# Kernel tuning notes

Measured on AMD Instinct MI355X. Metric: run time of the kernel, lower is better.

## Reference

```python
import jax, jax.numpy as jnp
import numpy as np

B, I, O = 8192, 512, 512

def setup_inputs() -> dict:
    key = jax.random.key(0)
    k1, k2, k3, k4 = jax.random.split(key, 4)
    x = jax.random.normal(k1, (B, I), dtype=jnp.float32)
    # per-edge polynomial activation params: f_ij(t) = w1*t + w2*t^2 + w3*t^3 + b
    edge_w = jax.random.normal(k2, (I, O, 3), dtype=jnp.float32) * 0.1
    edge_b = jax.random.normal(k3, (I, O), dtype=jnp.float32) * 0.1
    # xavier-uniform combination weights
    limit = float(np.sqrt(6.0 / (I + O)))
    comb_w = jax.random.uniform(k4, (I, O), dtype=jnp.float32, minval=-limit, maxval=limit)
    return {"x": x, "edge_w": edge_w, "edge_b": edge_b, "comb_w": comb_w}

def reference(x, edge_w, edge_b, comb_w):
    # basis: [B, I, 3] = (t, t^2, t^3)
    basis = jnp.stack([x, x * x, x * x * x], axis=-1)
    # out[b,o] = sum_i comb_w[i,o] * (sum_k basis[b,i,k]*edge_w[i,o,k] + edge_b[i,o])
    # fused to avoid materializing [B, I, O]
    w_eff = edge_w * comb_w[:, :, None]            # [I, O, 3]
    out = jnp.einsum('bik,iok->bo', basis, w_eff)  # [B, O]
    out = out + jnp.sum(comb_w * edge_b, axis=0)   # bias term, [O]
    return out
```

## Files before the change

kernel.cpp:

```cpp
#include <hip/hip_runtime.h>
#include <hip/hip_bf16.h>
#include <stdint.h>


static constexpr int ON_ = 512;

typedef __bf16 bf16x8 __attribute__((ext_vector_type(8)));
typedef float  f32x4  __attribute__((ext_vector_type(4)));

__device__ __forceinline__ unsigned int f2bf(float f) {
    unsigned int u = __float_as_uint(f);
    return ((u + 0x7FFFu + ((u >> 16) & 1u)) >> 16);
}

__global__ __launch_bounds__(256) void pack_all(const float* __restrict__ x,
                                                const float* __restrict__ edge_w,
                                                const float* __restrict__ comb_w,
                                                const float* __restrict__ edge_b,
                                                uint4* __restrict__ Xpk,
                                                uint4* __restrict__ Bpk,
                                                float* __restrict__ bias) {
    int bb = blockIdx.x;
    if (bb < 2048) {
        int id = bb * 256 + threadIdx.x;
        int l  = id & 63;
        int w  = id >> 6;
        int g  = w & 15;
        int rb = w >> 4;
        int r  = rb * 16 + (l & 15);
        int c  = g * 32 + ((l >> 4) << 3);
        const float4* xp = (const float4*)(x + (size_t)r * 512 + c);
        float4 v0 = xp[0], v1 = xp[1];
        uint4 o;
        o.x = f2bf(v0.x) | (f2bf(v0.y) << 16);
        o.y = f2bf(v0.z) | (f2bf(v0.w) << 16);
        o.z = f2bf(v1.x) | (f2bf(v1.y) << 16);
        o.w = f2bf(v1.z) | (f2bf(v1.w) << 16);
        Xpk[(size_t)w * 64 + l] = o;
    } else if (bb < 2176) {
        int id = (bb - 2048) * 256 + threadIdx.x;
        int l  = id & 63;
        int t  = id >> 6;
        int g  = t & 15;
        int cb = t >> 4;
        int o  = cb * 16 + (l & 15);
        int i0 = g * 32 + ((l >> 4) << 3);
        unsigned int w[3][4];
#pragma unroll
        for (int j = 0; j < 4; ++j) {
            int ia = i0 + 2 * j, ic = ia + 1;
            float ca = comb_w[(size_t)ia * ON_ + o];
            float cc = comb_w[(size_t)ic * ON_ + o];
            const float* ea = edge_w + ((size_t)ia * ON_ + o) * 3;
            const float* ec = edge_w + ((size_t)ic * ON_ + o) * 3;
#pragma unroll
            for (int p = 0; p < 3; ++p)
                w[p][j] = f2bf(ea[p] * ca) | (f2bf(ec[p] * cc) << 16);
        }
        size_t base = ((size_t)cb * 48 + g * 3) * 64 + l;
        Bpk[base]       = make_uint4(w[0][0], w[0][1], w[0][2], w[0][3]);
        Bpk[base + 64]  = make_uint4(w[1][0], w[1][1], w[1][2], w[1][3]);
        Bpk[base + 128] = make_uint4(w[2][0], w[2][1], w[2][2], w[2][3]);
    } else {
        __shared__ float red[4][64];
        int bo = bb - 2176;
        int tt = threadIdx.x;
        int o  = bo * 64 + (tt & 63);
        int iseg = tt >> 6;
        float s = 0.f;
        int ib = iseg * 128;
#pragma unroll 4
        for (int i = ib; i < ib + 128; ++i)
            s += comb_w[(size_t)i * ON_ + o] * edge_b[(size_t)i * ON_ + o];
        red[iseg][tt & 63] = s;
        __syncthreads();
        if (tt < 64)
            bias[bo * 64 + tt] = red[0][tt] + red[1][tt] + red[2][tt] + red[3][tt];
    }
}

#define PM(CAm, MI, CB0_, CB1_, CB2_, CB3_, CB4_, CB5_) do {                           \
    bf16x8 a1_ = __builtin_bit_cast(bf16x8, (CAm));                                    \
    float e0_ = __uint_as_float((CAm).x << 16), e1_ = __uint_as_float((CAm).x & 0xffff0000u); \
    float e2_ = __uint_as_float((CAm).y << 16), e3_ = __uint_as_float((CAm).y & 0xffff0000u); \
    float e4_ = __uint_as_float((CAm).z << 16), e5_ = __uint_as_float((CAm).z & 0xffff0000u); \
    float e6_ = __uint_as_float((CAm).w << 16), e7_ = __uint_as_float((CAm).w & 0xffff0000u); \
    float q0_ = e0_*e0_, q1_ = e1_*e1_, q2_ = e2_*e2_, q3_ = e3_*e3_;                  \
    float q4_ = e4_*e4_, q5_ = e5_*e5_, q6_ = e6_*e6_, q7_ = e7_*e7_;                  \
    bf16x8 a2_ = (bf16x8){ (__bf16)q0_, (__bf16)q1_, (__bf16)q2_, (__bf16)q3_,         \
                           (__bf16)q4_, (__bf16)q5_, (__bf16)q6_, (__bf16)q7_ };       \
    bf16x8 a3_ = (bf16x8){ (__bf16)(q0_*e0_), (__bf16)(q1_*e1_), (__bf16)(q2_*e2_), (__bf16)(q3_*e3_), \
                           (__bf16)(q4_*e4_), (__bf16)(q5_*e5_), (__bf16)(q6_*e6_), (__bf16)(q7_*e7_) }; \
    acc[MI][0] = __builtin_amdgcn_mfma_f32_16x16x32_bf16(a1_, __builtin_bit_cast(bf16x8, CB0_), acc[MI][0], 0, 0, 0); \
    acc[MI][1] = __builtin_amdgcn_mfma_f32_16x16x32_bf16(a1_, __builtin_bit_cast(bf16x8, CB3_), acc[MI][1], 0, 0, 0); \
    acc[MI][0] = __builtin_amdgcn_mfma_f32_16x16x32_bf16(a2_, __builtin_bit_cast(bf16x8, CB1_), acc[MI][0], 0, 0, 0); \
    acc[MI][1] = __builtin_amdgcn_mfma_f32_16x16x32_bf16(a2_, __builtin_bit_cast(bf16x8, CB4_), acc[MI][1], 0, 0, 0); \
    acc[MI][0] = __builtin_amdgcn_mfma_f32_16x16x32_bf16(a3_, __builtin_bit_cast(bf16x8, CB2_), acc[MI][0], 0, 0, 0); \
    acc[MI][1] = __builtin_amdgcn_mfma_f32_16x16x32_bf16(a3_, __builtin_bit_cast(bf16x8, CB5_), acc[MI][1], 0, 0, 0); \
} while (0)

#define STEP(PREF, CA0,CA1,CA2,CA3, CB0,CB1,CB2,CB3,CB4,CB5,                           \
                   NA0,NA1,NA2,NA3, NB0,NB1,NB2,NB3,NB4,NB5, WAITS) do {               \
    if (PREF) {                                                                        \
        NA0 = *(const uint4*)(pa0); NA1 = *(const uint4*)(pa1);                        \
        NA2 = *(const uint4*)(pa2); NA3 = *(const uint4*)(pa3);                        \
        NB0 = *(const uint4*)(pb0);        NB1 = *(const uint4*)(pb0 + 1024);          \
        NB2 = *(const uint4*)(pb0 + 2048); NB3 = *(const uint4*)(pb1);                 \
        NB4 = *(const uint4*)(pb1 + 1024); NB5 = *(const uint4*)(pb1 + 2048);          \
        pa0 += 1024; pa1 += 1024; pa2 += 1024; pa3 += 1024;                            \
        pb0 += 3072; pb1 += 3072;                                                      \
    }                                                                                  \
    asm volatile("s_waitcnt " WAITS ::: "memory");                                     \
    PM(CA0, 0, CB0, CB1, CB2, CB3, CB4, CB5);                                          \
    PM(CA1, 1, CB0, CB1, CB2, CB3, CB4, CB5);                                          \
    PM(CA2, 2, CB0, CB1, CB2, CB3, CB4, CB5);                                          \
    PM(CA3, 3, CB0, CB1, CB2, CB3, CB4, CB5);                                          \
} while (0)

__global__ __launch_bounds__(256, 2) void gemm_fused(const char* __restrict__ Xpk,
                                                     const char* __restrict__ Bpk,
                                                     const float* __restrict__ bias,
                                                     float* __restrict__ out) {
    const int tid = threadIdx.x;
    const int l   = tid & 63;
    const int wid = tid >> 6;
    const int wr  = wid >> 1, wc = wid & 1;

    int d  = blockIdx.x;
    int w  = (d & 7) * 64 + (d >> 3);
    int bx = w >> 3, by = w & 7;

    const char* pa0 = Xpk + ((size_t)(bx * 8 + wr * 4) * 16) * 1024 + (l << 4);
    const char* pa1 = pa0 + 16 * 1024;
    const char* pa2 = pa0 + 32 * 1024;
    const char* pa3 = pa0 + 48 * 1024;
    const char* pb0 = Bpk + ((size_t)(by * 4 + wc * 2) * 48) * 1024 + (l << 4);
    const char* pb1 = pb0 + 48 * 1024;

    f32x4 acc[4][2] = {};
    uint4 cA0, cA1, cA2, cA3, cB0, cB1, cB2, cB3, cB4, cB5;
    uint4 nA0, nA1, nA2, nA3, nB0, nB1, nB2, nB3, nB4, nB5;

    cA0 = *(const uint4*)(pa0); cA1 = *(const uint4*)(pa1);
    cA2 = *(const uint4*)(pa2); cA3 = *(const uint4*)(pa3);
    cB0 = *(const uint4*)(pb0);        cB1 = *(const uint4*)(pb0 + 1024);
    cB2 = *(const uint4*)(pb0 + 2048); cB3 = *(const uint4*)(pb1);
    cB4 = *(const uint4*)(pb1 + 1024); cB5 = *(const uint4*)(pb1 + 2048);
    pa0 += 1024; pa1 += 1024; pa2 += 1024; pa3 += 1024;
    pb0 += 3072; pb1 += 3072;

    for (int gp = 0; gp < 7; ++gp) {
        STEP(true, cA0,cA1,cA2,cA3, cB0,cB1,cB2,cB3,cB4,cB5,
                   nA0,nA1,nA2,nA3, nB0,nB1,nB2,nB3,nB4,nB5, "vmcnt(10)");
        STEP(true, nA0,nA1,nA2,nA3, nB0,nB1,nB2,nB3,nB4,nB5,
                   cA0,cA1,cA2,cA3, cB0,cB1,cB2,cB3,cB4,cB5, "vmcnt(10)");
    }
    STEP(true,  cA0,cA1,cA2,cA3, cB0,cB1,cB2,cB3,cB4,cB5,
                nA0,nA1,nA2,nA3, nB0,nB1,nB2,nB3,nB4,nB5, "vmcnt(10)");
    STEP(false, nA0,nA1,nA2,nA3, nB0,nB1,nB2,nB3,nB4,nB5,
                cA0,cA1,cA2,cA3, cB0,cB1,cB2,cB3,cB4,cB5, "vmcnt(0)");

    int lr = l >> 4, lc = l & 15;
#pragma unroll
    for (int n = 0; n < 2; ++n) {
        int o = (by << 6) + (wc << 5) + (n << 4) + lc;
        float bv = bias[o];
#pragma unroll
        for (int m = 0; m < 4; ++m) {
            int r0 = (bx << 7) + (wr << 6) + (m << 4) + (lr << 2);
#pragma unroll
            for (int j = 0; j < 4; ++j)
                out[(size_t)(r0 + j) * ON_ + o] = acc[m][n][j] + bv;
        }
    }
}

extern "C" void kernel_launch(void* const* d_in, const int* in_sizes, int n_in,
                              void* d_out, int out_size, void* d_ws, size_t ws_size,
                              hipStream_t stream) {
    const float* x      = (const float*)d_in[0];
    const float* edge_w = (const float*)d_in[1];
    const float* edge_b = (const float*)d_in[2];
    const float* comb_w = (const float*)d_in[3];
    float* out = (float*)d_out;

    char* ws = (char*)d_ws;
    char* Xpk   = ws;
    char* Bpk   = ws + 8388608;
    float* bias = (float*)(ws + 8388608 + 1572864);

    hipLaunchKernelGGL(pack_all, dim3(2048 + 128 + 8), dim3(256), 0, stream,
                       x, edge_w, comb_w, edge_b, (uint4*)Xpk, (uint4*)Bpk, bias);
    hipLaunchKernelGGL(gemm_fused, dim3(512), dim3(256), 0, stream, Xpk, Bpk, bias, out);
}
```

Measured before the change: 40.43 us.

## Deepen GEMM prefetch to triple-buffered registers and reorder MFMA issue

```diff
diff --git a/kernel.cpp b/kernel.cpp
--- a/kernel.cpp
+++ b/kernel.cpp
@@ -79,43 +79,66 @@
     }
 }
 
-#define PM(CAm, MI, CB0_, CB1_, CB2_, CB3_, CB4_, CB5_) do {                           \
-    bf16x8 a1_ = __builtin_bit_cast(bf16x8, (CAm));                                    \
-    float e0_ = __uint_as_float((CAm).x << 16), e1_ = __uint_as_float((CAm).x & 0xffff0000u); \
-    float e2_ = __uint_as_float((CAm).y << 16), e3_ = __uint_as_float((CAm).y & 0xffff0000u); \
-    float e4_ = __uint_as_float((CAm).z << 16), e5_ = __uint_as_float((CAm).z & 0xffff0000u); \
-    float e6_ = __uint_as_float((CAm).w << 16), e7_ = __uint_as_float((CAm).w & 0xffff0000u); \
-    float q0_ = e0_*e0_, q1_ = e1_*e1_, q2_ = e2_*e2_, q3_ = e3_*e3_;                  \
-    float q4_ = e4_*e4_, q5_ = e5_*e5_, q6_ = e6_*e6_, q7_ = e7_*e7_;                  \
-    bf16x8 a2_ = (bf16x8){ (__bf16)q0_, (__bf16)q1_, (__bf16)q2_, (__bf16)q3_,         \
-                           (__bf16)q4_, (__bf16)q5_, (__bf16)q6_, (__bf16)q7_ };       \
-    bf16x8 a3_ = (bf16x8){ (__bf16)(q0_*e0_), (__bf16)(q1_*e1_), (__bf16)(q2_*e2_), (__bf16)(q3_*e3_), \
-                           (__bf16)(q4_*e4_), (__bf16)(q5_*e5_), (__bf16)(q6_*e6_), (__bf16)(q7_*e7_) }; \
-    acc[MI][0] = __builtin_amdgcn_mfma_f32_16x16x32_bf16(a1_, __builtin_bit_cast(bf16x8, CB0_), acc[MI][0], 0, 0, 0); \
-    acc[MI][1] = __builtin_amdgcn_mfma_f32_16x16x32_bf16(a1_, __builtin_bit_cast(bf16x8, CB3_), acc[MI][1], 0, 0, 0); \
-    acc[MI][0] = __builtin_amdgcn_mfma_f32_16x16x32_bf16(a2_, __builtin_bit_cast(bf16x8, CB1_), acc[MI][0], 0, 0, 0); \
-    acc[MI][1] = __builtin_amdgcn_mfma_f32_16x16x32_bf16(a2_, __builtin_bit_cast(bf16x8, CB4_), acc[MI][1], 0, 0, 0); \
-    acc[MI][0] = __builtin_amdgcn_mfma_f32_16x16x32_bf16(a3_, __builtin_bit_cast(bf16x8, CB2_), acc[MI][0], 0, 0, 0); \
-    acc[MI][1] = __builtin_amdgcn_mfma_f32_16x16x32_bf16(a3_, __builtin_bit_cast(bf16x8, CB5_), acc[MI][1], 0, 0, 0); \
+__device__ __forceinline__ void ext_sq(const uint4 a, float* e, float* q) {
+    e[0] = __uint_as_float(a.x << 16); e[1] = __uint_as_float(a.x & 0xffff0000u);
+    e[2] = __uint_as_float(a.y << 16); e[3] = __uint_as_float(a.y & 0xffff0000u);
+    e[4] = __uint_as_float(a.z << 16); e[5] = __uint_as_float(a.z & 0xffff0000u);
+    e[6] = __uint_as_float(a.w << 16); e[7] = __uint_as_float(a.w & 0xffff0000u);
+#pragma unroll
+    for (int i = 0; i < 8; ++i) q[i] = e[i] * e[i];
+}
+
+#define MFMA_ROW(F0, F1, F2, F3, BN0, BN1) do {                                           \
+    bf16x8 b0_ = __builtin_bit_cast(bf16x8, BN0);                                         \
+    bf16x8 b1_ = __builtin_bit_cast(bf16x8, BN1);                                         \
+    acc[0][0] = __builtin_amdgcn_mfma_f32_16x16x32_bf16(F0, b0_, acc[0][0], 0, 0, 0);      \
+    acc[1][0] = __builtin_amdgcn_mfma_f32_16x16x32_bf16(F1, b0_, acc[1][0], 0, 0, 0);      \
+    acc[2][0] = __builtin_amdgcn_mfma_f32_16x16x32_bf16(F2, b0_, acc[2][0], 0, 0, 0);      \
+    acc[3][0] = __builtin_amdgcn_mfma_f32_16x16x32_bf16(F3, b0_, acc[3][0], 0, 0, 0);      \
+    acc[0][1] = __builtin_amdgcn_mfma_f32_16x16x32_bf16(F0, b1_, acc[0][1], 0, 0, 0);      \
+    acc[1][1] = __builtin_amdgcn_mfma_f32_16x16x32_bf16(F1, b1_, acc[1][1], 0, 0, 0);      \
+    acc[2][1] = __builtin_amdgcn_mfma_f32_16x16x32_bf16(F2, b1_, acc[2][1], 0, 0, 0);      \
+    acc[3][1] = __builtin_amdgcn_mfma_f32_16x16x32_bf16(F3, b1_, acc[3][1], 0, 0, 0);      \
 } while (0)
 
-#define STEP(PREF, CA0,CA1,CA2,CA3, CB0,CB1,CB2,CB3,CB4,CB5,                           \
-                   NA0,NA1,NA2,NA3, NB0,NB1,NB2,NB3,NB4,NB5, WAITS) do {               \
-    if (PREF) {                                                                        \
-        NA0 = *(const uint4*)(pa0); NA1 = *(const uint4*)(pa1);                        \
-        NA2 = *(const uint4*)(pa2); NA3 = *(const uint4*)(pa3);                        \
-        NB0 = *(const uint4*)(pb0);        NB1 = *(const uint4*)(pb0 + 1024);          \
-        NB2 = *(const uint4*)(pb0 + 2048); NB3 = *(const uint4*)(pb1);                 \
-        NB4 = *(const uint4*)(pb1 + 1024); NB5 = *(const uint4*)(pb1 + 2048);          \
-        pa0 += 1024; pa1 += 1024; pa2 += 1024; pa3 += 1024;                            \
-        pb0 += 3072; pb1 += 3072;                                                      \
-    }                                                                                  \
-    asm volatile("s_waitcnt " WAITS ::: "memory");                                     \
-    PM(CA0, 0, CB0, CB1, CB2, CB3, CB4, CB5);                                          \
-    PM(CA1, 1, CB0, CB1, CB2, CB3, CB4, CB5);                                          \
-    PM(CA2, 2, CB0, CB1, CB2, CB3, CB4, CB5);                                          \
-    PM(CA3, 3, CB0, CB1, CB2, CB3, CB4, CB5);                                          \
+#define COMP(A0, A1, A2, A3, B0, B1, B2, B3, B4, B5) do {                                  \
+    bf16x8 f0_ = __builtin_bit_cast(bf16x8, A0), f1_ = __builtin_bit_cast(bf16x8, A1);     \
+    bf16x8 f2_ = __builtin_bit_cast(bf16x8, A2), f3_ = __builtin_bit_cast(bf16x8, A3);     \
+    MFMA_ROW(f0_, f1_, f2_, f3_, B0, B3);                                                  \
+    float e0_[8], q0_[8], e1_[8], q1_[8], e2_[8], q2_[8], e3_[8], q3_[8];                  \
+    ext_sq(A0, e0_, q0_); ext_sq(A1, e1_, q1_);                                            \
+    ext_sq(A2, e2_, q2_); ext_sq(A3, e3_, q3_);                                            \
+    bf16x8 s0_ = (bf16x8){ (__bf16)q0_[0], (__bf16)q0_[1], (__bf16)q0_[2], (__bf16)q0_[3], \
+                           (__bf16)q0_[4], (__bf16)q0_[5], (__bf16)q0_[6], (__bf16)q0_[7] };\
+    bf16x8 s1_ = (bf16x8){ (__bf16)q1_[0], (__bf16)q1_[1], (__bf16)q1_[2], (__bf16)q1_[3], \
+                           (__bf16)q1_[4], (__bf16)q1_[5], (__bf16)q1_[6], (__bf16)q1_[7] };\
+    bf16x8 s2_ = (bf16x8){ (__bf16)q2_[0], (__bf16)q2_[1], (__bf16)q2_[2], (__bf16)q2_[3], \
+                           (__bf16)q2_[4], (__bf16)q2_[5], (__bf16)q2_[6], (__bf16)q2_[7] };\
+    bf16x8 s3_ = (bf16x8){ (__bf16)q3_[0], (__bf16)q3_[1], (__bf16)q3_[2], (__bf16)q3_[3], \
+                           (__bf16)q3_[4], (__bf16)q3_[5], (__bf16)q3_[6], (__bf16)q3_[7] };\
+    MFMA_ROW(s0_, s1_, s2_, s3_, B1, B4);                                                  \
+    bf16x8 c0_ = (bf16x8){ (__bf16)(q0_[0]*e0_[0]), (__bf16)(q0_[1]*e0_[1]), (__bf16)(q0_[2]*e0_[2]), (__bf16)(q0_[3]*e0_[3]), \
+                           (__bf16)(q0_[4]*e0_[4]), (__bf16)(q0_[5]*e0_[5]), (__bf16)(q0_[6]*e0_[6]), (__bf16)(q0_[7]*e0_[7]) }; \
+    bf16x8 c1_ = (bf16x8){ (__bf16)(q1_[0]*e1_[0]), (__bf16)(q1_[1]*e1_[1]), (__bf16)(q1_[2]*e1_[2]), (__bf16)(q1_[3]*e1_[3]), \
+                           (__bf16)(q1_[4]*e1_[4]), (__bf16)(q1_[5]*e1_[5]), (__bf16)(q1_[6]*e1_[6]), (__bf16)(q1_[7]*e1_[7]) }; \
+    bf16x8 c2_ = (bf16x8){ (__bf16)(q2_[0]*e2_[0]), (__bf16)(q2_[1]*e2_[1]), (__bf16)(q2_[2]*e2_[2]), (__bf16)(q2_[3]*e2_[3]), \
+                           (__bf16)(q2_[4]*e2_[4]), (__bf16)(q2_[5]*e2_[5]), (__bf16)(q2_[6]*e2_[6]), (__bf16)(q2_[7]*e2_[7]) }; \
+    bf16x8 c3_ = (bf16x8){ (__bf16)(q3_[0]*e3_[0]), (__bf16)(q3_[1]*e3_[1]), (__bf16)(q3_[2]*e3_[2]), (__bf16)(q3_[3]*e3_[3]), \
+                           (__bf16)(q3_[4]*e3_[4]), (__bf16)(q3_[5]*e3_[5]), (__bf16)(q3_[6]*e3_[6]), (__bf16)(q3_[7]*e3_[7]) }; \
+    MFMA_ROW(c0_, c1_, c2_, c3_, B2, B5);                                                  \
 } while (0)
+
+#define LOADG(B0, B1, B2, B3, B4, B5, B6, B7, B8, B9) do {                                 \
+    B0 = *(const uint4*)(pa0); B1 = *(const uint4*)(pa1);                                  \
+    B2 = *(const uint4*)(pa2); B3 = *(const uint4*)(pa3);                                  \
+    B4 = *(const uint4*)(pb0);        B5 = *(const uint4*)(pb0 + 1024);                    \
+    B6 = *(const uint4*)(pb0 + 2048); B7 = *(const uint4*)(pb1);                           \
+    B8 = *(const uint4*)(pb1 + 1024); B9 = *(const uint4*)(pb1 + 2048);                    \
+    pa0 += 1024; pa1 += 1024; pa2 += 1024; pa3 += 1024;                                    \
+    pb0 += 3072; pb1 += 3072;                                                              \
+} while (0)
+
+#define WAITV(N) asm volatile("s_waitcnt vmcnt(" #N ")" ::: "memory")
 
 __global__ __launch_bounds__(256, 2) void gemm_fused(const char* __restrict__ Xpk,
                                                      const char* __restrict__ Bpk,
@@ -138,27 +161,35 @@
     const char* pb1 = pb0 + 48 * 1024;
 
     f32x4 acc[4][2] = {};
-    uint4 cA0, cA1, cA2, cA3, cB0, cB1, cB2, cB3, cB4, cB5;
-    uint4 nA0, nA1, nA2, nA3, nB0, nB1, nB2, nB3, nB4, nB5;
-
-    cA0 = *(const uint4*)(pa0); cA1 = *(const uint4*)(pa1);
-    cA2 = *(const uint4*)(pa2); cA3 = *(const uint4*)(pa3);
-    cB0 = *(const uint4*)(pb0);        cB1 = *(const uint4*)(pb0 + 1024);
-    cB2 = *(const uint4*)(pb0 + 2048); cB3 = *(const uint4*)(pb1);
-    cB4 = *(const uint4*)(pb1 + 1024); cB5 = *(const uint4*)(pb1 + 2048);
-    pa0 += 1024; pa1 += 1024; pa2 += 1024; pa3 += 1024;
-    pb0 += 3072; pb1 += 3072;
-
-    for (int gp = 0; gp < 7; ++gp) {
-        STEP(true, cA0,cA1,cA2,cA3, cB0,cB1,cB2,cB3,cB4,cB5,
-                   nA0,nA1,nA2,nA3, nB0,nB1,nB2,nB3,nB4,nB5, "vmcnt(10)");
-        STEP(true, nA0,nA1,nA2,nA3, nB0,nB1,nB2,nB3,nB4,nB5,
-                   cA0,cA1,cA2,cA3, cB0,cB1,cB2,cB3,cB4,cB5, "vmcnt(10)");
+    uint4 u0, u1, u2, u3, u4, u5, u6, u7, u8, u9;
+    uint4 v0, v1, v2, v3, v4, v5, v6, v7, v8, v9;
+    uint4 w0, w1, w2, w3, w4, w5, w6, w7, w8, w9;
+
+    LOADG(u0, u1, u2, u3, u4, u5, u6, u7, u8, u9);
+    LOADG(v0, v1, v2, v3, v4, v5, v6, v7, v8, v9);
+
+#pragma unroll 1
+    for (int tr = 0; tr < 4; ++tr) {
+        LOADG(w0, w1, w2, w3, w4, w5, w6, w7, w8, w9);
+        WAITV(20);
+        COMP(u0, u1, u2, u3, u4, u5, u6, u7, u8, u9);
+        LOADG(u0, u1, u2, u3, u4, u5, u6, u7, u8, u9);
+        WAITV(20);
+        COMP(v0, v1, v2, v3, v4, v5, v6, v7, v8, v9);
+        LOADG(v0, v1, v2, v3, v4, v5, v6, v7, v8, v9);
+        WAITV(20);
+        COMP(w0, w1, w2, w3, w4, w5, w6, w7, w8, w9);
     }
-    STEP(true,  cA0,cA1,cA2,cA3, cB0,cB1,cB2,cB3,cB4,cB5,
-                nA0,nA1,nA2,nA3, nB0,nB1,nB2,nB3,nB4,nB5, "vmcnt(10)");
-    STEP(false, nA0,nA1,nA2,nA3, nB0,nB1,nB2,nB3,nB4,nB5,
-                cA0,cA1,cA2,cA3, cB0,cB1,cB2,cB3,cB4,cB5, "vmcnt(0)");
+    LOADG(w0, w1, w2, w3, w4, w5, w6, w7, w8, w9);
+    WAITV(20);
+    COMP(u0, u1, u2, u3, u4, u5, u6, u7, u8, u9);
+    LOADG(u0, u1, u2, u3, u4, u5, u6, u7, u8, u9);
+    WAITV(20);
+    COMP(v0, v1, v2, v3, v4, v5, v6, v7, v8, v9);
+    WAITV(10);
+    COMP(w0, w1, w2, w3, w4, w5, w6, w7, w8, w9);
+    WAITV(0);
+    COMP(u0, u1, u2, u3, u4, u5, u6, u7, u8, u9);
 
     int lr = l >> 4, lc = l & 15;
 #pragma unroll
```

Result: no change. 40.26 us (-0.4%).

## Halve GEMM block tile rows, double grid, raise occupancy to four blocks

Applied to the files above, without the earlier changes.

```diff
diff --git a/kernel.cpp b/kernel.cpp
--- a/kernel.cpp
+++ b/kernel.cpp
@@ -79,45 +79,48 @@
     }
 }
 
-#define PM(CAm, MI, CB0_, CB1_, CB2_, CB3_, CB4_, CB5_) do {                           \
-    bf16x8 a1_ = __builtin_bit_cast(bf16x8, (CAm));                                    \
-    float e0_ = __uint_as_float((CAm).x << 16), e1_ = __uint_as_float((CAm).x & 0xffff0000u); \
-    float e2_ = __uint_as_float((CAm).y << 16), e3_ = __uint_as_float((CAm).y & 0xffff0000u); \
-    float e4_ = __uint_as_float((CAm).z << 16), e5_ = __uint_as_float((CAm).z & 0xffff0000u); \
-    float e6_ = __uint_as_float((CAm).w << 16), e7_ = __uint_as_float((CAm).w & 0xffff0000u); \
-    float q0_ = e0_*e0_, q1_ = e1_*e1_, q2_ = e2_*e2_, q3_ = e3_*e3_;                  \
-    float q4_ = e4_*e4_, q5_ = e5_*e5_, q6_ = e6_*e6_, q7_ = e7_*e7_;                  \
-    bf16x8 a2_ = (bf16x8){ (__bf16)q0_, (__bf16)q1_, (__bf16)q2_, (__bf16)q3_,         \
-                           (__bf16)q4_, (__bf16)q5_, (__bf16)q6_, (__bf16)q7_ };       \
-    bf16x8 a3_ = (bf16x8){ (__bf16)(q0_*e0_), (__bf16)(q1_*e1_), (__bf16)(q2_*e2_), (__bf16)(q3_*e3_), \
-                           (__bf16)(q4_*e4_), (__bf16)(q5_*e5_), (__bf16)(q6_*e6_), (__bf16)(q7_*e7_) }; \
-    acc[MI][0] = __builtin_amdgcn_mfma_f32_16x16x32_bf16(a1_, __builtin_bit_cast(bf16x8, CB0_), acc[MI][0], 0, 0, 0); \
-    acc[MI][1] = __builtin_amdgcn_mfma_f32_16x16x32_bf16(a1_, __builtin_bit_cast(bf16x8, CB3_), acc[MI][1], 0, 0, 0); \
-    acc[MI][0] = __builtin_amdgcn_mfma_f32_16x16x32_bf16(a2_, __builtin_bit_cast(bf16x8, CB1_), acc[MI][0], 0, 0, 0); \
-    acc[MI][1] = __builtin_amdgcn_mfma_f32_16x16x32_bf16(a2_, __builtin_bit_cast(bf16x8, CB4_), acc[MI][1], 0, 0, 0); \
-    acc[MI][0] = __builtin_amdgcn_mfma_f32_16x16x32_bf16(a3_, __builtin_bit_cast(bf16x8, CB2_), acc[MI][0], 0, 0, 0); \
-    acc[MI][1] = __builtin_amdgcn_mfma_f32_16x16x32_bf16(a3_, __builtin_bit_cast(bf16x8, CB5_), acc[MI][1], 0, 0, 0); \
+#define STRIP(Am, MI, BP0, BP1, BP2, BQ0, BQ1, BQ2) do {                                   \
+    bf16x8 a1_ = __builtin_bit_cast(bf16x8, Am);                                           \
+    acc[MI][0] = __builtin_amdgcn_mfma_f32_16x16x32_bf16(a1_, __builtin_bit_cast(bf16x8, BP0), acc[MI][0], 0, 0, 0); \
+    acc[MI][1] = __builtin_amdgcn_mfma_f32_16x16x32_bf16(a1_, __builtin_bit_cast(bf16x8, BQ0), acc[MI][1], 0, 0, 0); \
+    float e0_ = __uint_as_float((Am).x << 16), e1_ = __uint_as_float((Am).x & 0xffff0000u); \
+    float e2_ = __uint_as_float((Am).y << 16), e3_ = __uint_as_float((Am).y & 0xffff0000u); \
+    float e4_ = __uint_as_float((Am).z << 16), e5_ = __uint_as_float((Am).z & 0xffff0000u); \
+    float e6_ = __uint_as_float((Am).w << 16), e7_ = __uint_as_float((Am).w & 0xffff0000u); \
+    float q0_ = e0_*e0_, q1_ = e1_*e1_, q2_ = e2_*e2_, q3_ = e3_*e3_;                      \
+    float q4_ = e4_*e4_, q5_ = e5_*e5_, q6_ = e6_*e6_, q7_ = e7_*e7_;                      \
+    bf16x8 s_ = (bf16x8){ (__bf16)q0_, (__bf16)q1_, (__bf16)q2_, (__bf16)q3_,              \
+                          (__bf16)q4_, (__bf16)q5_, (__bf16)q6_, (__bf16)q7_ };            \
+    acc[MI][0] = __builtin_amdgcn_mfma_f32_16x16x32_bf16(s_, __builtin_bit_cast(bf16x8, BP1), acc[MI][0], 0, 0, 0); \
+    acc[MI][1] = __builtin_amdgcn_mfma_f32_16x16x32_bf16(s_, __builtin_bit_cast(bf16x8, BQ1), acc[MI][1], 0, 0, 0); \
+    bf16x8 c_ = (bf16x8){ (__bf16)(q0_*e0_), (__bf16)(q1_*e1_), (__bf16)(q2_*e2_), (__bf16)(q3_*e3_), \
+                          (__bf16)(q4_*e4_), (__bf16)(q5_*e5_), (__bf16)(q6_*e6_), (__bf16)(q7_*e7_) }; \
+    acc[MI][0] = __builtin_amdgcn_mfma_f32_16x16x32_bf16(c_, __builtin_bit_cast(bf16x8, BP2), acc[MI][0], 0, 0, 0); \
+    acc[MI][1] = __builtin_amdgcn_mfma_f32_16x16x32_bf16(c_, __builtin_bit_cast(bf16x8, BQ2), acc[MI][1], 0, 0, 0); \
 } while (0)
 
-#define STEP(PREF, CA0,CA1,CA2,CA3, CB0,CB1,CB2,CB3,CB4,CB5,                           \
-                   NA0,NA1,NA2,NA3, NB0,NB1,NB2,NB3,NB4,NB5, WAITS) do {               \
-    if (PREF) {                                                                        \
-        NA0 = *(const uint4*)(pa0); NA1 = *(const uint4*)(pa1);                        \
-        NA2 = *(const uint4*)(pa2); NA3 = *(const uint4*)(pa3);                        \
-        NB0 = *(const uint4*)(pb0);        NB1 = *(const uint4*)(pb0 + 1024);          \
-        NB2 = *(const uint4*)(pb0 + 2048); NB3 = *(const uint4*)(pb1);                 \
-        NB4 = *(const uint4*)(pb1 + 1024); NB5 = *(const uint4*)(pb1 + 2048);          \
-        pa0 += 1024; pa1 += 1024; pa2 += 1024; pa3 += 1024;                            \
-        pb0 += 3072; pb1 += 3072;                                                      \
-    }                                                                                  \
-    asm volatile("s_waitcnt " WAITS ::: "memory");                                     \
-    PM(CA0, 0, CB0, CB1, CB2, CB3, CB4, CB5);                                          \
-    PM(CA1, 1, CB0, CB1, CB2, CB3, CB4, CB5);                                          \
-    PM(CA2, 2, CB0, CB1, CB2, CB3, CB4, CB5);                                          \
-    PM(CA3, 3, CB0, CB1, CB2, CB3, CB4, CB5);                                          \
+#define COMP8(S0, S1, S2, S3, S4, S5, S6, S7) do {                                         \
+    STRIP(S0, 0, S2, S3, S4, S5, S6, S7);                                                  \
+    STRIP(S1, 1, S2, S3, S4, S5, S6, S7);                                                  \
 } while (0)
 
-__global__ __launch_bounds__(256, 2) void gemm_fused(const char* __restrict__ Xpk,
+#define LOADG8(S0, S1, S2, S3, S4, S5, S6, S7) do {                                        \
+    S0 = *(const uint4*)(pa0); S1 = *(const uint4*)(pa1);                                  \
+    S2 = *(const uint4*)(pb0);        S3 = *(const uint4*)(pb0 + 1024);                    \
+    S4 = *(const uint4*)(pb0 + 2048); S5 = *(const uint4*)(pb1);                           \
+    S6 = *(const uint4*)(pb1 + 1024); S7 = *(const uint4*)(pb1 + 2048);                    \
+    pa0 += 1024; pa1 += 1024; pb0 += 3072; pb1 += 3072;                                    \
+} while (0)
+
+#define WAITV(N) asm volatile("s_waitcnt vmcnt(" #N ")" ::: "memory")
+
+#define STEP8(C0,C1,C2,C3,C4,C5,C6,C7, N0,N1,N2,N3,N4,N5,N6,N7) do {                       \
+    LOADG8(N0,N1,N2,N3,N4,N5,N6,N7);                                                       \
+    WAITV(8);                                                                              \
+    COMP8(C0,C1,C2,C3,C4,C5,C6,C7);                                                        \
+} while (0)
+
+__global__ __launch_bounds__(256, 4) void gemm_fused(const char* __restrict__ Xpk,
                                                      const char* __restrict__ Bpk,
                                                      const float* __restrict__ bias,
                                                      float* __restrict__ out) {
@@ -127,38 +130,28 @@
     const int wr  = wid >> 1, wc = wid & 1;
 
     int d  = blockIdx.x;
-    int w  = (d & 7) * 64 + (d >> 3);
+    int w  = (d & 7) * 128 + (d >> 3);
     int bx = w >> 3, by = w & 7;
 
-    const char* pa0 = Xpk + ((size_t)(bx * 8 + wr * 4) * 16) * 1024 + (l << 4);
+    const char* pa0 = Xpk + ((size_t)(bx * 4 + wr * 2) * 16) * 1024 + (l << 4);
     const char* pa1 = pa0 + 16 * 1024;
-    const char* pa2 = pa0 + 32 * 1024;
-    const char* pa3 = pa0 + 48 * 1024;
     const char* pb0 = Bpk + ((size_t)(by * 4 + wc * 2) * 48) * 1024 + (l << 4);
     const char* pb1 = pb0 + 48 * 1024;
 
-    f32x4 acc[4][2] = {};
-    uint4 cA0, cA1, cA2, cA3, cB0, cB1, cB2, cB3, cB4, cB5;
-    uint4 nA0, nA1, nA2, nA3, nB0, nB1, nB2, nB3, nB4, nB5;
+    f32x4 acc[2][2] = {};
+    uint4 u0, u1, u2, u3, u4, u5, u6, u7;
+    uint4 v0, v1, v2, v3, v4, v5, v6, v7;
 
-    cA0 = *(const uint4*)(pa0); cA1 = *(const uint4*)(pa1);
-    cA2 = *(const uint4*)(pa2); cA3 = *(const uint4*)(pa3);
-    cB0 = *(const uint4*)(pb0);        cB1 = *(const uint4*)(pb0 + 1024);
-    cB2 = *(const uint4*)(pb0 + 2048); cB3 = *(const uint4*)(pb1);
-    cB4 = *(const uint4*)(pb1 + 1024); cB5 = *(const uint4*)(pb1 + 2048);
-    pa0 += 1024; pa1 += 1024; pa2 += 1024; pa3 += 1024;
-    pb0 += 3072; pb1 += 3072;
+    LOADG8(u0, u1, u2, u3, u4, u5, u6, u7);
 
-    for (int gp = 0; gp < 7; ++gp) {
-        STEP(true, cA0,cA1,cA2,cA3, cB0,cB1,cB2,cB3,cB4,cB5,
-                   nA0,nA1,nA2,nA3, nB0,nB1,nB2,nB3,nB4,nB5, "vmcnt(10)");
-        STEP(true, nA0,nA1,nA2,nA3, nB0,nB1,nB2,nB3,nB4,nB5,
-                   cA0,cA1,cA2,cA3, cB0,cB1,cB2,cB3,cB4,cB5, "vmcnt(10)");
+#pragma unroll 1
+    for (int tr = 0; tr < 7; ++tr) {
+        STEP8(u0,u1,u2,u3,u4,u5,u6,u7, v0,v1,v2,v3,v4,v5,v6,v7);
+        STEP8(v0,v1,v2,v3,v4,v5,v6,v7, u0,u1,u2,u3,u4,u5,u6,u7);
     }
-    STEP(true,  cA0,cA1,cA2,cA3, cB0,cB1,cB2,cB3,cB4,cB5,
-                nA0,nA1,nA2,nA3, nB0,nB1,nB2,nB3,nB4,nB5, "vmcnt(10)");
-    STEP(false, nA0,nA1,nA2,nA3, nB0,nB1,nB2,nB3,nB4,nB5,
-                cA0,cA1,cA2,cA3, cB0,cB1,cB2,cB3,cB4,cB5, "vmcnt(0)");
+    STEP8(u0,u1,u2,u3,u4,u5,u6,u7, v0,v1,v2,v3,v4,v5,v6,v7);
+    WAITV(0);
+    COMP8(v0,v1,v2,v3,v4,v5,v6,v7);
 
     int lr = l >> 4, lc = l & 15;
 #pragma unroll
@@ -166,8 +159,8 @@
         int o = (by << 6) + (wc << 5) + (n << 4) + lc;
         float bv = bias[o];
 #pragma unroll
-        for (int m = 0; m < 4; ++m) {
-            int r0 = (bx << 7) + (wr << 6) + (m << 4) + (lr << 2);
+        for (int m = 0; m < 2; ++m) {
+            int r0 = (bx << 6) + (wr << 5) + (m << 4) + (lr << 2);
 #pragma unroll
             for (int j = 0; j < 4; ++j)
                 out[(size_t)(r0 + j) * ON_ + o] = acc[m][n][j] + bv;
@@ -191,5 +184,5 @@
 
     hipLaunchKernelGGL(pack_all, dim3(2048 + 128 + 8), dim3(256), 0, stream,
                        x, edge_w, comb_w, edge_b, (uint4*)Xpk, (uint4*)Bpk, bias);
-    hipLaunchKernelGGL(gemm_fused, dim3(512), dim3(256), 0, stream, Xpk, Bpk, bias, out);
+    hipLaunchKernelGGL(gemm_fused, dim3(1024), dim3(256), 0, stream, Xpk, Bpk, bias, out);
 }
```

Result: slower. 42.11 us (+4.2%).
